# Performance work log

Measured on AMD Instinct MI355X. Metric: run time of the kernel, lower is better.

Reference implementation:

```python
import jax, jax.numpy as jnp
import numpy as np

N = 50000   # nodes
E = 800000  # edges (avg degree 16)
F = 128     # node_features


def setup_inputs() -> dict:
    key = jax.random.key(0)
    ks = jax.random.split(key, 10)
    s = 1.0 / np.sqrt(F)
    x = jax.random.normal(ks[0], (N, F), jnp.float32)
    edge_index = jax.random.randint(ks[1], (2, E), 0, N, dtype=jnp.int32)
    edge_weight = jax.random.uniform(ks[2], (E,), jnp.float32)
    # EvolveGCNO initial weight (glorot-ish) and GRU parameters (PyTorch layout)
    W0 = jax.random.uniform(ks[3], (F, F), jnp.float32, -s, s)
    W_ih = jax.random.uniform(ks[4], (3 * F, F), jnp.float32, -s, s)
    W_hh = jax.random.uniform(ks[5], (3 * F, F), jnp.float32, -s, s)
    b_ih = jax.random.uniform(ks[6], (3 * F,), jnp.float32, -s, s)
    b_hh = jax.random.uniform(ks[7], (3 * F,), jnp.float32, -s, s)
    # Linear(F, 1) head
    w_lin = jax.random.uniform(ks[8], (1, F), jnp.float32, -s, s)
    b_lin = jax.random.uniform(ks[9], (1,), jnp.float32, -s, s)
    return dict(x=x, edge_index=edge_index, edge_weight=edge_weight, W0=W0,
                W_ih=W_ih, W_hh=W_hh, b_ih=b_ih, b_hh=b_hh,
                w_lin=w_lin, b_lin=b_lin)


def _gru_evolve(W0, W_ih, W_hh, b_ih, b_hh):
    # GRU(input=W0, hidden=W0): seq_len=1, batch=F, feature=F (PyTorch gate order r,z,n)
    gi = W0 @ W_ih.T + b_ih  # [F, 3F]
    gh = W0 @ W_hh.T + b_hh  # [F, 3F]
    f = W0.shape[1]
    i_r, i_z, i_n = gi[:, :f], gi[:, f:2 * f], gi[:, 2 * f:]
    h_r, h_z, h_n = gh[:, :f], gh[:, f:2 * f], gh[:, 2 * f:]
    r = jax.nn.sigmoid(i_r + h_r)
    z = jax.nn.sigmoid(i_z + h_z)
    n = jnp.tanh(i_n + r * h_n)
    return (1.0 - z) * n + z * W0  # evolved weight [F, F]


def reference(x, edge_index, edge_weight, W0, W_ih, W_hh, b_ih, b_hh, w_lin, b_lin):
    n_nodes = x.shape[0]
    W = _gru_evolve(W0, W_ih, W_hh, b_ih, b_hh)
    # gcn_norm: add self loops (weight 1), symmetric D^-1/2 A D^-1/2
    loop = jnp.arange(n_nodes, dtype=edge_index.dtype)
    src = jnp.concatenate([edge_index[0], loop])
    dst = jnp.concatenate([edge_index[1], loop])
    w = jnp.concatenate([edge_weight, jnp.ones((n_nodes,), x.dtype)])
    deg = jax.ops.segment_sum(w, dst, num_segments=n_nodes)
    dinv = jnp.where(deg > 0, jax.lax.rsqrt(deg), 0.0)
    norm = dinv[src] * w * dinv[dst]  # [E+N]
    xw = x @ W  # [N, F]
    h = jax.ops.segment_sum(norm[:, None] * xw[src], dst, num_segments=n_nodes)
    h = jnp.tanh(h)
    return h @ w_lin.T + b_lin  # [N, 1]
```

## Files before the change

kernel.cpp:

```cpp
#include <hip/hip_runtime.h>
#include <hip/hip_bf16.h>
#include <math.h>

#define N_NODES 50000
#define N_EDGES 800000
#define FDIM 128
#define SCAN_BLOCKS 196
#define XW_BLOCKS 391

typedef unsigned int uint32;
typedef __attribute__((ext_vector_type(8))) __bf16 bf16x8;
typedef __attribute__((ext_vector_type(8))) short short8;
typedef __attribute__((ext_vector_type(16))) float f32x16;

#define FLAG_A 200
#define FLAG_B 201
#define SCANNED 256

__device__ inline unsigned short f2bf(float f) {
  unsigned int u = __float_as_uint(f);
  unsigned int r = u + 0x7fffu + ((u >> 16) & 1u);
  return (unsigned short)(r >> 16);
}

__global__ __launch_bounds__(384) void evolve_kernel(
    const float* __restrict__ W0, const float* __restrict__ Wih,
    const float* __restrict__ Whh, const float* __restrict__ bih,
    const float* __restrict__ bhh, float* __restrict__ W,
    int* __restrict__ cnt, int* __restrict__ part) {
  int i = blockIdx.x;
  int jj = threadIdx.x;
  int gid = i * 384 + jj;
  for (int j = gid; j < N_NODES; j += 128 * 384) cnt[j] = 0;
  if (gid == 0) part[FLAG_A] = 0;
  if (gid == 1) part[FLAG_B] = 0;

  __shared__ float w0s[FDIM];
  __shared__ float gis[3 * FDIM];
  __shared__ float ghs[3 * FDIM];
  if (jj < FDIM) w0s[jj] = W0[i * FDIM + jj];
  __syncthreads();
  float gi = bih[jj], gh = bhh[jj];
  const float4* wih4 = (const float4*)(Wih + jj * FDIM);
  const float4* whh4 = (const float4*)(Whh + jj * FDIM);
#pragma unroll 8
  for (int k = 0; k < FDIM / 4; k++) {
    float4 a = wih4[k];
    float4 b = whh4[k];
    float w0a = w0s[4 * k], w0b = w0s[4 * k + 1];
    float w0c = w0s[4 * k + 2], w0d = w0s[4 * k + 3];
    gi += a.x * w0a + a.y * w0b + a.z * w0c + a.w * w0d;
    gh += b.x * w0a + b.y * w0b + b.z * w0c + b.w * w0d;
  }
  gis[jj] = gi;
  ghs[jj] = gh;
  __syncthreads();
  if (jj < FDIM) {
    float r = 1.0f / (1.0f + expf(-(gis[jj] + ghs[jj])));
    float z = 1.0f / (1.0f + expf(-(gis[jj + FDIM] + ghs[jj + FDIM])));
    float nn = tanhf(gis[jj + 2 * FDIM] + r * ghs[jj + 2 * FDIM]);
    W[i * FDIM + jj] = (1.0f - z) * nn + z * w0s[jj];
  }
}

__global__ __launch_bounds__(256) void histxw_kernel(
    const int* __restrict__ ei, int* __restrict__ cnt, int* __restrict__ rank,
    const float* __restrict__ x, const float* __restrict__ W,
    unsigned short* __restrict__ y, int n) {
  __shared__ short Bs[16 * 128 * 8];
  int t = threadIdx.x;
  if (blockIdx.x >= XW_BLOCKS) {
    int idx = (blockIdx.x - XW_BLOCKS) * 256 + t;
    if (idx < N_EDGES) {
      int dst = ei[N_EDGES + idx];
      rank[idx] = atomicAdd(&cnt[dst], 1);
    }
    return;
  }
#pragma unroll
  for (int i = 0; i < 64; i++) {
    int idx = i * 256 + t;
    int k = idx >> 7, nn = idx & 127;
    Bs[(((k >> 3) << 7) + nn) * 8 + (k & 7)] = (short)f2bf(W[idx]);
  }
  __syncthreads();

  int lane = t & 63;
  int wid = blockIdx.x * 4 + (t >> 6);
  int tr = wid * 32;
  if (tr >= n) return;
  int m = lane & 31;
  int q2 = lane >> 5;

  int row = tr + m;
  if (row >= n) row = n - 1;
  const float* xr = x + (size_t)row * FDIM;

  bf16x8 a[8];
#pragma unroll
  for (int kc = 0; kc < 8; kc++) {
    int k0 = kc * 16 + q2 * 8;
    float4 p = *(const float4*)(xr + k0);
    float4 q = *(const float4*)(xr + k0 + 4);
    short8 s;
    s[0] = (short)f2bf(p.x); s[1] = (short)f2bf(p.y);
    s[2] = (short)f2bf(p.z); s[3] = (short)f2bf(p.w);
    s[4] = (short)f2bf(q.x); s[5] = (short)f2bf(q.y);
    s[6] = (short)f2bf(q.z); s[7] = (short)f2bf(q.w);
    a[kc] = __builtin_bit_cast(bf16x8, s);
  }

  f32x16 acc[4];
#pragma unroll
  for (int ct = 0; ct < 4; ct++) {
#pragma unroll
    for (int r = 0; r < 16; r++) acc[ct][r] = 0.0f;
  }
#pragma unroll
  for (int ct = 0; ct < 4; ct++) {
    int nn = ct * 32 + m;
#pragma unroll
    for (int kc = 0; kc < 8; kc++) {
      int kg = kc * 2 + q2;
      bf16x8 b = __builtin_bit_cast(
          bf16x8, *(const short8*)(Bs + (((kg << 7) + nn) << 3)));
      acc[ct] = __builtin_amdgcn_mfma_f32_32x32x16_bf16(a[kc], b, acc[ct], 0,
                                                        0, 0);
    }
  }

#pragma unroll
  for (int r = 0; r < 16; r++) {
    int rl = (r & 3) + ((r >> 2) << 3) + (q2 << 2);
    int rg = tr + rl;
    if (rg < n) {
#pragma unroll
      for (int ct = 0; ct < 4; ct++) {
        y[(size_t)rg * FDIM + ct * 32 + m] = f2bf(acc[ct][r]);
      }
    }
  }
}

__global__ __launch_bounds__(256) void scan_all_kernel(
    const int* __restrict__ cnt, int* __restrict__ part, int* __restrict__ offs,
    int n) {
  __shared__ int tmp[256];
  int t = threadIdx.x;
  int bid = blockIdx.x;
  int idx = bid * 256 + t;
  int v = (idx < n) ? cnt[idx] : 0;
  tmp[t] = v;
  __syncthreads();
#pragma unroll
  for (int off = 1; off < 256; off <<= 1) {
    int u = (t >= off) ? tmp[t - off] : 0;
    __syncthreads();
    tmp[t] += u;
    __syncthreads();
  }
  int local_excl = tmp[t] - v;
  int block_sum = tmp[255];
  if (t == 0) {
    __hip_atomic_store(&part[bid], block_sum, __ATOMIC_RELEASE,
                       __HIP_MEMORY_SCOPE_AGENT);
    __hip_atomic_fetch_add(&part[FLAG_A], 1, __ATOMIC_ACQ_REL,
                           __HIP_MEMORY_SCOPE_AGENT);
  }
  if (bid == 0) {
    if (t == 0) {
      while (__hip_atomic_load(&part[FLAG_A], __ATOMIC_ACQUIRE,
                               __HIP_MEMORY_SCOPE_AGENT) < SCAN_BLOCKS) {
        __builtin_amdgcn_s_sleep(1);
      }
    }
    __syncthreads();
    __shared__ int ps[256];
    int pv = (t < SCAN_BLOCKS)
                 ? __hip_atomic_load(&part[t], __ATOMIC_RELAXED,
                                     __HIP_MEMORY_SCOPE_AGENT)
                 : 0;
    ps[t] = pv;
    __syncthreads();
#pragma unroll
    for (int off = 1; off < 256; off <<= 1) {
      int u = (t >= off) ? ps[t - off] : 0;
      __syncthreads();
      ps[t] += u;
      __syncthreads();
    }
    if (t < SCAN_BLOCKS)
      __hip_atomic_store(&part[SCANNED + t], ps[t] - pv, __ATOMIC_RELAXED,
                         __HIP_MEMORY_SCOPE_AGENT);
    __syncthreads();
    if (t == 0)
      __hip_atomic_store(&part[FLAG_B], 1, __ATOMIC_RELEASE,
                         __HIP_MEMORY_SCOPE_AGENT);
  }
  if (t == 0) {
    while (__hip_atomic_load(&part[FLAG_B], __ATOMIC_ACQUIRE,
                             __HIP_MEMORY_SCOPE_AGENT) == 0) {
      __builtin_amdgcn_s_sleep(1);
    }
  }
  __syncthreads();
  int base = __hip_atomic_load(&part[SCANNED + bid], __ATOMIC_RELAXED,
                               __HIP_MEMORY_SCOPE_AGENT);
  int excl = base + local_excl;
  if (idx < n) offs[idx] = excl;
  if (idx == n - 1) offs[n] = excl + v;
}

__global__ void scatter_kernel(const int* __restrict__ ei,
                               const float* __restrict__ ew,
                               const int* __restrict__ offs,
                               const int* __restrict__ rank,
                               int2* __restrict__ csr, int e) {
  int idx = blockIdx.x * blockDim.x + threadIdx.x;
  if (idx < e) {
    int src = ei[idx];
    int dst = ei[N_EDGES + idx];
    int pos = offs[dst] + rank[idx];
    csr[pos] = make_int2(src, __float_as_int(ew[idx]));
  }
}

__global__ __launch_bounds__(256) void deg_dinv_kernel(
    const int2* __restrict__ csr, const int* __restrict__ offs,
    float* __restrict__ dinv, int n) {
  int i = blockIdx.x * blockDim.x + threadIdx.x;
  if (i >= n) return;
  int b = offs[i], e = offs[i + 1];
  float d = 1.0f;
  for (int j = b; j < e; j++) d += __int_as_float(csr[j].y);
  dinv[i] = (d > 0.0f) ? rsqrtf(d) : 0.0f;
}

__global__ __launch_bounds__(256) void gather_kernel(
    const uint32* __restrict__ yb, const int* __restrict__ offs,
    const int2* __restrict__ csr, const float* __restrict__ dinv,
    const float* __restrict__ wl, const float* __restrict__ bl,
    float* __restrict__ out, int n) {
  int wid = (int)((blockIdx.x * (size_t)blockDim.x + threadIdx.x) >> 6);
  int lane = threadIdx.x & 63;
  if (wid >= n) return;
  float di = dinv[wid];
  uint32 uv = yb[(size_t)wid * 64 + lane];
  float ax = di * __uint_as_float(uv << 16);
  float ay = di * __uint_as_float(uv & 0xffff0000u);
  int beg = offs[wid], end = offs[wid + 1];
  int e = beg;
  for (; e + 4 <= end; e += 4) {
    int2 c0 = csr[e];
    int2 c1 = csr[e + 1];
    int2 c2 = csr[e + 2];
    int2 c3 = csr[e + 3];
    uint32 u0 = yb[(size_t)c0.x * 64 + lane];
    uint32 u1 = yb[(size_t)c1.x * 64 + lane];
    uint32 u2 = yb[(size_t)c2.x * 64 + lane];
    uint32 u3 = yb[(size_t)c3.x * 64 + lane];
    float w0 = __int_as_float(c0.y) * dinv[c0.x];
    float w1 = __int_as_float(c1.y) * dinv[c1.x];
    float w2 = __int_as_float(c2.y) * dinv[c2.x];
    float w3 = __int_as_float(c3.y) * dinv[c3.x];
    ax += w0 * __uint_as_float(u0 << 16);
    ay += w0 * __uint_as_float(u0 & 0xffff0000u);
    ax += w1 * __uint_as_float(u1 << 16);
    ay += w1 * __uint_as_float(u1 & 0xffff0000u);
    ax += w2 * __uint_as_float(u2 << 16);
    ay += w2 * __uint_as_float(u2 & 0xffff0000u);
    ax += w3 * __uint_as_float(u3 << 16);
    ay += w3 * __uint_as_float(u3 & 0xffff0000u);
  }
  for (; e < end; e++) {
    int2 c = csr[e];
    uint32 u = yb[(size_t)c.x * 64 + lane];
    float wn = __int_as_float(c.y) * dinv[c.x];
    ax += wn * __uint_as_float(u << 16);
    ay += wn * __uint_as_float(u & 0xffff0000u);
  }
  float2 wv = ((const float2*)wl)[lane];
  float p = tanhf(di * ax) * wv.x + tanhf(di * ay) * wv.y;
#pragma unroll
  for (int o = 32; o > 0; o >>= 1) p += __shfl_down(p, o, 64);
  if (lane == 0) out[wid] = p + bl[0];
}

extern "C" void kernel_launch(void* const* d_in, const int* in_sizes, int n_in,
                              void* d_out, int out_size, void* d_ws,
                              size_t ws_size, hipStream_t stream) {
  const float* x = (const float*)d_in[0];
  const int* ei = (const int*)d_in[1];
  const float* ew = (const float*)d_in[2];
  const float* W0 = (const float*)d_in[3];
  const float* Wih = (const float*)d_in[4];
  const float* Whh = (const float*)d_in[5];
  const float* bih = (const float*)d_in[6];
  const float* bhh = (const float*)d_in[7];
  const float* wl = (const float*)d_in[8];
  const float* bl = (const float*)d_in[9];
  float* out = (float*)d_out;

  float* ws = (float*)d_ws;
  float* W_ev = ws;
  unsigned short* y = (unsigned short*)(W_ev + 16384);
  float* dinv = (float*)(y + (size_t)N_NODES * FDIM);
  int* cnt = (int*)(dinv + N_NODES);
  int* rank = cnt + N_NODES;
  int* offs = rank + N_EDGES;
  int2* csr = (int2*)(offs + 50004);
  int* part = (int*)(csr + N_EDGES);

  evolve_kernel<<<FDIM, 384, 0, stream>>>(W0, Wih, Whh, bih, bhh, W_ev, cnt,
                                          part);
  histxw_kernel<<<XW_BLOCKS + (N_EDGES + 255) / 256, 256, 0, stream>>>(
      ei, cnt, rank, x, W_ev, y, N_NODES);
  scan_all_kernel<<<SCAN_BLOCKS, 256, 0, stream>>>(cnt, part, offs, N_NODES);
  scatter_kernel<<<(N_EDGES + 255) / 256, 256, 0, stream>>>(ei, ew, offs, rank,
                                                            csr, N_EDGES);
  deg_dinv_kernel<<<(N_NODES + 255) / 256, 256, 0, stream>>>(csr, offs, dinv,
                                                             N_NODES);
  gather_kernel<<<(N_NODES * 64) / 256, 256, 0, stream>>>(
      (const uint32*)y, offs, csr, dinv, wl, bl, out, N_NODES);
}
```

Measured before the change: 213.7 us.

## Fuse degree, scan and scatter into one kernel and prenormalize CSR weights

Edge degrees are now accumulated with float atomics during the histogram pass. Scan and scatter are fused into one kernel behind a grid-wide barrier, and the deg_dinv kernel is removed. CSR weights are pre-multiplied by dinv[src], and the gather loads CSR entries cooperatively across the wavefront and broadcasts them with shuffles, so it no longer issues a dinv lookup per edge. The evolved weight is written already converted to bf16 in the MFMA layout, so histxw only does a vector copy. This removes two launches and redundant memory traffic, at the cost of float atomics that make degree summation order non-deterministic and a spin barrier that assumes all 196 scan blocks are resident at once.

```diff
diff --git a/kernel.cpp b/kernel.cpp
--- a/kernel.cpp
+++ b/kernel.cpp
@@ -15,6 +15,7 @@
 
 #define FLAG_A 200
 #define FLAG_B 201
+#define FLAG_C 202
 #define SCANNED 256
 
 __device__ inline unsigned short f2bf(float f) {
@@ -26,14 +27,16 @@
 __global__ __launch_bounds__(384) void evolve_kernel(
     const float* __restrict__ W0, const float* __restrict__ Wih,
     const float* __restrict__ Whh, const float* __restrict__ bih,
-    const float* __restrict__ bhh, float* __restrict__ W,
-    int* __restrict__ cnt, int* __restrict__ part) {
+    const float* __restrict__ bhh, unsigned short* __restrict__ Wbf,
+    int* __restrict__ cnt, float* __restrict__ degf, int* __restrict__ part) {
   int i = blockIdx.x;
   int jj = threadIdx.x;
   int gid = i * 384 + jj;
-  for (int j = gid; j < N_NODES; j += 128 * 384) cnt[j] = 0;
-  if (gid == 0) part[FLAG_A] = 0;
-  if (gid == 1) part[FLAG_B] = 0;
+  for (int j = gid; j < N_NODES; j += 128 * 384) {
+    cnt[j] = 0;
+    degf[j] = 0.0f;
+  }
+  if (gid < 3) part[FLAG_A + gid] = 0;
 
   __shared__ float w0s[FDIM];
   __shared__ float gis[3 * FDIM];
@@ -59,13 +62,15 @@
     float r = 1.0f / (1.0f + expf(-(gis[jj] + ghs[jj])));
     float z = 1.0f / (1.0f + expf(-(gis[jj + FDIM] + ghs[jj + FDIM])));
     float nn = tanhf(gis[jj + 2 * FDIM] + r * ghs[jj + 2 * FDIM]);
-    W[i * FDIM + jj] = (1.0f - z) * nn + z * w0s[jj];
+    float val = (1.0f - z) * nn + z * w0s[jj];
+    Wbf[((((i >> 3) << 7) + jj) << 3) + (i & 7)] = f2bf(val);
   }
 }
 
 __global__ __launch_bounds__(256) void histxw_kernel(
-    const int* __restrict__ ei, int* __restrict__ cnt, int* __restrict__ rank,
-    const float* __restrict__ x, const float* __restrict__ W,
+    const int* __restrict__ ei, const float* __restrict__ ew,
+    int* __restrict__ cnt, float* __restrict__ degf, int* __restrict__ rank,
+    const float* __restrict__ x, const unsigned short* __restrict__ Wbf,
     unsigned short* __restrict__ y, int n) {
   __shared__ short Bs[16 * 128 * 8];
   int t = threadIdx.x;
@@ -74,14 +79,13 @@
     if (idx < N_EDGES) {
       int dst = ei[N_EDGES + idx];
       rank[idx] = atomicAdd(&cnt[dst], 1);
+      unsafeAtomicAdd(&degf[dst], ew[idx]);
     }
     return;
   }
 #pragma unroll
-  for (int i = 0; i < 64; i++) {
-    int idx = i * 256 + t;
-    int k = idx >> 7, nn = idx & 127;
-    Bs[(((k >> 3) << 7) + nn) * 8 + (k & 7)] = (short)f2bf(W[idx]);
+  for (int i = 0; i < 8; i++) {
+    ((short8*)Bs)[i * 256 + t] = ((const short8*)Wbf)[i * 256 + t];
   }
   __syncthreads();
 
@@ -142,13 +146,17 @@
   }
 }
 
-__global__ __launch_bounds__(256) void scan_all_kernel(
-    const int* __restrict__ cnt, int* __restrict__ part, int* __restrict__ offs,
-    int n) {
+__global__ __launch_bounds__(256) void scan_scatter_kernel(
+    const int* __restrict__ cnt, const float* __restrict__ degf,
+    int* __restrict__ part, int* __restrict__ offs, float* __restrict__ dinv,
+    const int* __restrict__ ei, const float* __restrict__ ew,
+    const int* __restrict__ rank, int2* __restrict__ csr) {
   __shared__ int tmp[256];
   int t = threadIdx.x;
   int bid = blockIdx.x;
   int idx = bid * 256 + t;
+  int n = N_NODES;
+  if (idx < n) dinv[idx] = rsqrtf(degf[idx] + 1.0f);
   int v = (idx < n) ? cnt[idx] : 0;
   tmp[t] = v;
   __syncthreads();
@@ -209,31 +217,25 @@
   int excl = base + local_excl;
   if (idx < n) offs[idx] = excl;
   if (idx == n - 1) offs[n] = excl + v;
-}
-
-__global__ void scatter_kernel(const int* __restrict__ ei,
-                               const float* __restrict__ ew,
-                               const int* __restrict__ offs,
-                               const int* __restrict__ rank,
-                               int2* __restrict__ csr, int e) {
-  int idx = blockIdx.x * blockDim.x + threadIdx.x;
-  if (idx < e) {
-    int src = ei[idx];
-    int dst = ei[N_EDGES + idx];
-    int pos = offs[dst] + rank[idx];
-    csr[pos] = make_int2(src, __float_as_int(ew[idx]));
-  }
-}
-
-__global__ __launch_bounds__(256) void deg_dinv_kernel(
-    const int2* __restrict__ csr, const int* __restrict__ offs,
-    float* __restrict__ dinv, int n) {
-  int i = blockIdx.x * blockDim.x + threadIdx.x;
-  if (i >= n) return;
-  int b = offs[i], e = offs[i + 1];
-  float d = 1.0f;
-  for (int j = b; j < e; j++) d += __int_as_float(csr[j].y);
-  dinv[i] = (d > 0.0f) ? rsqrtf(d) : 0.0f;
+
+  __syncthreads();
+  if (t == 0) {
+    __hip_atomic_fetch_add(&part[FLAG_C], 1, __ATOMIC_ACQ_REL,
+                           __HIP_MEMORY_SCOPE_AGENT);
+    while (__hip_atomic_load(&part[FLAG_C], __ATOMIC_ACQUIRE,
+                             __HIP_MEMORY_SCOPE_AGENT) < SCAN_BLOCKS) {
+      __builtin_amdgcn_s_sleep(1);
+    }
+  }
+  __syncthreads();
+
+  for (int e = idx; e < N_EDGES; e += SCAN_BLOCKS * 256) {
+    int src = ei[e];
+    int dst = ei[N_EDGES + e];
+    int pos = offs[dst] + rank[e];
+    float wn = ew[e] * dinv[src];
+    csr[pos] = make_int2(src, __float_as_int(wn));
+  }
 }
 
 __global__ __launch_bounds__(256) void gather_kernel(
@@ -249,35 +251,41 @@
   float ax = di * __uint_as_float(uv << 16);
   float ay = di * __uint_as_float(uv & 0xffff0000u);
   int beg = offs[wid], end = offs[wid + 1];
-  int e = beg;
-  for (; e + 4 <= end; e += 4) {
-    int2 c0 = csr[e];
-    int2 c1 = csr[e + 1];
-    int2 c2 = csr[e + 2];
-    int2 c3 = csr[e + 3];
-    uint32 u0 = yb[(size_t)c0.x * 64 + lane];
-    uint32 u1 = yb[(size_t)c1.x * 64 + lane];
-    uint32 u2 = yb[(size_t)c2.x * 64 + lane];
-    uint32 u3 = yb[(size_t)c3.x * 64 + lane];
-    float w0 = __int_as_float(c0.y) * dinv[c0.x];
-    float w1 = __int_as_float(c1.y) * dinv[c1.x];
-    float w2 = __int_as_float(c2.y) * dinv[c2.x];
-    float w3 = __int_as_float(c3.y) * dinv[c3.x];
-    ax += w0 * __uint_as_float(u0 << 16);
-    ay += w0 * __uint_as_float(u0 & 0xffff0000u);
-    ax += w1 * __uint_as_float(u1 << 16);
-    ay += w1 * __uint_as_float(u1 & 0xffff0000u);
-    ax += w2 * __uint_as_float(u2 << 16);
-    ay += w2 * __uint_as_float(u2 & 0xffff0000u);
-    ax += w3 * __uint_as_float(u3 << 16);
-    ay += w3 * __uint_as_float(u3 & 0xffff0000u);
-  }
-  for (; e < end; e++) {
-    int2 c = csr[e];
-    uint32 u = yb[(size_t)c.x * 64 + lane];
-    float wn = __int_as_float(c.y) * dinv[c.x];
-    ax += wn * __uint_as_float(u << 16);
-    ay += wn * __uint_as_float(u & 0xffff0000u);
+  for (int base = beg; base < end; base += 64) {
+    int mm = end - base;
+    if (mm > 64) mm = 64;
+    int2 c = make_int2(0, 0);
+    if (lane < mm) c = csr[base + lane];
+    int j = 0;
+    for (; j + 4 <= mm; j += 4) {
+      int s0 = __shfl(c.x, j);
+      int s1 = __shfl(c.x, j + 1);
+      int s2 = __shfl(c.x, j + 2);
+      int s3 = __shfl(c.x, j + 3);
+      float w0 = __uint_as_float((uint32)__shfl(c.y, j));
+      float w1 = __uint_as_float((uint32)__shfl(c.y, j + 1));
+      float w2 = __uint_as_float((uint32)__shfl(c.y, j + 2));
+      float w3 = __uint_as_float((uint32)__shfl(c.y, j + 3));
+      uint32 u0 = yb[(size_t)s0 * 64 + lane];
+      uint32 u1 = yb[(size_t)s1 * 64 + lane];
+      uint32 u2 = yb[(size_t)s2 * 64 + lane];
+      uint32 u3 = yb[(size_t)s3 * 64 + lane];
+      ax += w0 * __uint_as_float(u0 << 16);
+      ay += w0 * __uint_as_float(u0 & 0xffff0000u);
+      ax += w1 * __uint_as_float(u1 << 16);
+      ay += w1 * __uint_as_float(u1 & 0xffff0000u);
+      ax += w2 * __uint_as_float(u2 << 16);
+      ay += w2 * __uint_as_float(u2 & 0xffff0000u);
+      ax += w3 * __uint_as_float(u3 << 16);
+      ay += w3 * __uint_as_float(u3 & 0xffff0000u);
+    }
+    for (; j < mm; j++) {
+      int s = __shfl(c.x, j);
+      float wn = __uint_as_float((uint32)__shfl(c.y, j));
+      uint32 u = yb[(size_t)s * 64 + lane];
+      ax += wn * __uint_as_float(u << 16);
+      ay += wn * __uint_as_float(u & 0xffff0000u);
+    }
   }
   float2 wv = ((const float2*)wl)[lane];
   float p = tanhf(di * ax) * wv.x + tanhf(di * ay) * wv.y;
@@ -301,25 +309,22 @@
   const float* bl = (const float*)d_in[9];
   float* out = (float*)d_out;
 
-  float* ws = (float*)d_ws;
-  float* W_ev = ws;
-  unsigned short* y = (unsigned short*)(W_ev + 16384);
+  unsigned short* Wbf = (unsigned short*)d_ws;
+  unsigned short* y = Wbf + 16384;
   float* dinv = (float*)(y + (size_t)N_NODES * FDIM);
-  int* cnt = (int*)(dinv + N_NODES);
+  float* degf = dinv + N_NODES;
+  int* cnt = (int*)(degf + N_NODES);
   int* rank = cnt + N_NODES;
   int* offs = rank + N_EDGES;
   int2* csr = (int2*)(offs + 50004);
   int* part = (int*)(csr + N_EDGES);
 
-  evolve_kernel<<<FDIM, 384, 0, stream>>>(W0, Wih, Whh, bih, bhh, W_ev, cnt,
-                                          part);
+  evolve_kernel<<<FDIM, 384, 0, stream>>>(W0, Wih, Whh, bih, bhh, Wbf, cnt,
+                                          degf, part);
   histxw_kernel<<<XW_BLOCKS + (N_EDGES + 255) / 256, 256, 0, stream>>>(
-      ei, cnt, rank, x, W_ev, y, N_NODES);
-  scan_all_kernel<<<SCAN_BLOCKS, 256, 0, stream>>>(cnt, part, offs, N_NODES);
-  scatter_kernel<<<(N_EDGES + 255) / 256, 256, 0, stream>>>(ei, ew, offs, rank,
-                                                            csr, N_EDGES);
-  deg_dinv_kernel<<<(N_NODES + 255) / 256, 256, 0, stream>>>(csr, offs, dinv,
-                                                             N_NODES);
+      ei, ew, cnt, degf, rank, x, Wbf, y, N_NODES);
+  scan_scatter_kernel<<<SCAN_BLOCKS, 256, 0, stream>>>(cnt, degf, part, offs,
+                                                       dinv, ei, ew, rank, csr);
   gather_kernel<<<(N_NODES * 64) / 256, 256, 0, stream>>>(
       (const uint32*)y, offs, csr, dinv, wl, bl, out, N_NODES);
 }
```

Measured after the change: 253.3 us. +18.5%, slower.

## Replicate histogram counters and prepack evolved weight as bf16 in MFMA layout

Applied to the files above, without the earlier changes.

Splits the per-node edge counter into 8 replicas selected by block index, with each thread handling four edges via int4 loads and tagging its rank with the replica id. The scan sums the replicas and writes per-replica base offsets back, which scatter uses for placement. The evolve kernel now writes W directly as bf16 in the MFMA-friendly layout, and the xw blocks load it in two half-tiles, removing the per-block fp32-to-bf16 conversion and halving LDS use. This targets atomic contention on hot destinations and redundant conversion work, at the cost of 8x counter memory and the extra zeroing that goes with it.

```diff
diff --git a/kernel.cpp b/kernel.cpp
--- a/kernel.cpp
+++ b/kernel.cpp
@@ -7,6 +7,8 @@
 #define FDIM 128
 #define SCAN_BLOCKS 196
 #define XW_BLOCKS 391
+#define HIST_BLOCKS 782
+#define NREP 8
 
 typedef unsigned int uint32;
 typedef __attribute__((ext_vector_type(8))) __bf16 bf16x8;
@@ -26,14 +28,13 @@
 __global__ __launch_bounds__(384) void evolve_kernel(
     const float* __restrict__ W0, const float* __restrict__ Wih,
     const float* __restrict__ Whh, const float* __restrict__ bih,
-    const float* __restrict__ bhh, float* __restrict__ W,
-    int* __restrict__ cnt, int* __restrict__ part) {
+    const float* __restrict__ bhh, unsigned short* __restrict__ Wbf,
+    int* __restrict__ cnt_r, int* __restrict__ part) {
   int i = blockIdx.x;
   int jj = threadIdx.x;
   int gid = i * 384 + jj;
-  for (int j = gid; j < N_NODES; j += 128 * 384) cnt[j] = 0;
-  if (gid == 0) part[FLAG_A] = 0;
-  if (gid == 1) part[FLAG_B] = 0;
+  for (int j = gid; j < NREP * N_NODES; j += 128 * 384) cnt_r[j] = 0;
+  if (gid < 2) part[FLAG_A + gid] = 0;
 
   __shared__ float w0s[FDIM];
   __shared__ float gis[3 * FDIM];
@@ -59,36 +60,34 @@
     float r = 1.0f / (1.0f + expf(-(gis[jj] + ghs[jj])));
     float z = 1.0f / (1.0f + expf(-(gis[jj + FDIM] + ghs[jj + FDIM])));
     float nn = tanhf(gis[jj + 2 * FDIM] + r * ghs[jj + 2 * FDIM]);
-    W[i * FDIM + jj] = (1.0f - z) * nn + z * w0s[jj];
+    float val = (1.0f - z) * nn + z * w0s[jj];
+    Wbf[((((i >> 3) << 7) + jj) << 3) + (i & 7)] = f2bf(val);
   }
 }
 
 __global__ __launch_bounds__(256) void histxw_kernel(
-    const int* __restrict__ ei, int* __restrict__ cnt, int* __restrict__ rank,
-    const float* __restrict__ x, const float* __restrict__ W,
+    const int* __restrict__ ei, int* __restrict__ cnt_r, int* __restrict__ rank,
+    const float* __restrict__ x, const unsigned short* __restrict__ Wbf,
     unsigned short* __restrict__ y, int n) {
-  __shared__ short Bs[16 * 128 * 8];
+  __shared__ short Bs[8192];
   int t = threadIdx.x;
   if (blockIdx.x >= XW_BLOCKS) {
-    int idx = (blockIdx.x - XW_BLOCKS) * 256 + t;
-    if (idx < N_EDGES) {
-      int dst = ei[N_EDGES + idx];
-      rank[idx] = atomicAdd(&cnt[dst], 1);
+    int rep = blockIdx.x & (NREP - 1);
+    int e0 = (blockIdx.x - XW_BLOCKS) * 1024 + t * 4;
+    if (e0 < N_EDGES) {
+      int4 d4 = *(const int4*)(ei + N_EDGES + e0);
+      int tag = rep << 24;
+      int r0 = atomicAdd(&cnt_r[d4.x * NREP + rep], 1);
+      int r1 = atomicAdd(&cnt_r[d4.y * NREP + rep], 1);
+      int r2 = atomicAdd(&cnt_r[d4.z * NREP + rep], 1);
+      int r3 = atomicAdd(&cnt_r[d4.w * NREP + rep], 1);
+      *(int4*)(rank + e0) = make_int4(tag | r0, tag | r1, tag | r2, tag | r3);
     }
     return;
   }
-#pragma unroll
-  for (int i = 0; i < 64; i++) {
-    int idx = i * 256 + t;
-    int k = idx >> 7, nn = idx & 127;
-    Bs[(((k >> 3) << 7) + nn) * 8 + (k & 7)] = (short)f2bf(W[idx]);
-  }
-  __syncthreads();
-
   int lane = t & 63;
   int wid = blockIdx.x * 4 + (t >> 6);
   int tr = wid * 32;
-  if (tr >= n) return;
   int m = lane & 31;
   int q2 = lane >> 5;
 
@@ -116,16 +115,29 @@
 #pragma unroll
     for (int r = 0; r < 16; r++) acc[ct][r] = 0.0f;
   }
-#pragma unroll
-  for (int ct = 0; ct < 4; ct++) {
-    int nn = ct * 32 + m;
-#pragma unroll
-    for (int kc = 0; kc < 8; kc++) {
-      int kg = kc * 2 + q2;
-      bf16x8 b = __builtin_bit_cast(
-          bf16x8, *(const short8*)(Bs + (((kg << 7) + nn) << 3)));
-      acc[ct] = __builtin_amdgcn_mfma_f32_32x32x16_bf16(a[kc], b, acc[ct], 0,
-                                                        0, 0);
+
+#pragma unroll
+  for (int h = 0; h < 2; h++) {
+    __syncthreads();
+#pragma unroll
+    for (int i = 0; i < 4; i++) {
+      int li = i * 256 + t;
+      ((short8*)Bs)[li] =
+          ((const short8*)Wbf)[((li >> 6) << 7) + (h << 6) + (li & 63)];
+    }
+    __syncthreads();
+#pragma unroll
+    for (int cti = 0; cti < 2; cti++) {
+      int ct = h * 2 + cti;
+      int nnl = cti * 32 + m;
+#pragma unroll
+      for (int kc = 0; kc < 8; kc++) {
+        int kg = kc * 2 + q2;
+        bf16x8 b = __builtin_bit_cast(bf16x8,
+                                      ((const short8*)Bs)[(kg << 6) + nnl]);
+        acc[ct] = __builtin_amdgcn_mfma_f32_32x32x16_bf16(a[kc], b, acc[ct],
+                                                          0, 0, 0);
+      }
     }
   }
 
@@ -143,13 +155,22 @@
 }
 
 __global__ __launch_bounds__(256) void scan_all_kernel(
-    const int* __restrict__ cnt, int* __restrict__ part, int* __restrict__ offs,
+    int* __restrict__ cnt_r, int* __restrict__ part, int* __restrict__ offs,
     int n) {
   __shared__ int tmp[256];
   int t = threadIdx.x;
   int bid = blockIdx.x;
   int idx = bid * 256 + t;
-  int v = (idx < n) ? cnt[idx] : 0;
+  int c[NREP];
+  int v = 0;
+  if (idx < n) {
+    int4 a = *(const int4*)(cnt_r + idx * NREP);
+    int4 b = *(const int4*)(cnt_r + idx * NREP + 4);
+    c[0] = a.x; c[1] = a.y; c[2] = a.z; c[3] = a.w;
+    c[4] = b.x; c[5] = b.y; c[6] = b.z; c[7] = b.w;
+#pragma unroll
+    for (int r = 0; r < NREP; r++) v += c[r];
+  }
   tmp[t] = v;
   __syncthreads();
 #pragma unroll
@@ -207,20 +228,37 @@
   int base = __hip_atomic_load(&part[SCANNED + bid], __ATOMIC_RELAXED,
                                __HIP_MEMORY_SCOPE_AGENT);
   int excl = base + local_excl;
-  if (idx < n) offs[idx] = excl;
+  if (idx < n) {
+    offs[idx] = excl;
+    int run = excl;
+    int4 o0, o1;
+    o0.x = run; run += c[0];
+    o0.y = run; run += c[1];
+    o0.z = run; run += c[2];
+    o0.w = run; run += c[3];
+    o1.x = run; run += c[4];
+    o1.y = run; run += c[5];
+    o1.z = run; run += c[6];
+    o1.w = run;
+    *(int4*)(cnt_r + idx * NREP) = o0;
+    *(int4*)(cnt_r + idx * NREP + 4) = o1;
+  }
   if (idx == n - 1) offs[n] = excl + v;
 }
 
 __global__ void scatter_kernel(const int* __restrict__ ei,
                                const float* __restrict__ ew,
-                               const int* __restrict__ offs,
+                               const int* __restrict__ base_r,
                                const int* __restrict__ rank,
                                int2* __restrict__ csr, int e) {
   int idx = blockIdx.x * blockDim.x + threadIdx.x;
   if (idx < e) {
     int src = ei[idx];
     int dst = ei[N_EDGES + idx];
-    int pos = offs[dst] + rank[idx];
+    int rw = rank[idx];
+    int rep = ((uint32)rw) >> 24;
+    int loc = rw & 0xFFFFFF;
+    int pos = base_r[dst * NREP + rep] + loc;
     csr[pos] = make_int2(src, __float_as_int(ew[idx]));
   }
 }
@@ -301,23 +339,23 @@
   const float* bl = (const float*)d_in[9];
   float* out = (float*)d_out;
 
-  float* ws = (float*)d_ws;
-  float* W_ev = ws;
-  unsigned short* y = (unsigned short*)(W_ev + 16384);
+  unsigned short* Wbf = (unsigned short*)d_ws;
+  unsigned short* y = Wbf + 16384;
   float* dinv = (float*)(y + (size_t)N_NODES * FDIM);
-  int* cnt = (int*)(dinv + N_NODES);
-  int* rank = cnt + N_NODES;
+  int* cnt_r = (int*)(dinv + N_NODES);
+  int* rank = cnt_r + NREP * N_NODES;
   int* offs = rank + N_EDGES;
   int2* csr = (int2*)(offs + 50004);
   int* part = (int*)(csr + N_EDGES);
 
-  evolve_kernel<<<FDIM, 384, 0, stream>>>(W0, Wih, Whh, bih, bhh, W_ev, cnt,
+  evolve_kernel<<<FDIM, 384, 0, stream>>>(W0, Wih, Whh, bih, bhh, Wbf, cnt_r,
                                           part);
-  histxw_kernel<<<XW_BLOCKS + (N_EDGES + 255) / 256, 256, 0, stream>>>(
-      ei, cnt, rank, x, W_ev, y, N_NODES);
-  scan_all_kernel<<<SCAN_BLOCKS, 256, 0, stream>>>(cnt, part, offs, N_NODES);
-  scatter_kernel<<<(N_EDGES + 255) / 256, 256, 0, stream>>>(ei, ew, offs, rank,
-                                                            csr, N_EDGES);
+  histxw_kernel<<<XW_BLOCKS + HIST_BLOCKS, 256, 0, stream>>>(ei, cnt_r, rank,
+                                                             x, Wbf, y,
+                                                             N_NODES);
+  scan_all_kernel<<<SCAN_BLOCKS, 256, 0, stream>>>(cnt_r, part, offs, N_NODES);
+  scatter_kernel<<<(N_EDGES + 255) / 256, 256, 0, stream>>>(ei, ew, cnt_r,
+                                                            rank, csr, N_EDGES);
   deg_dinv_kernel<<<(N_NODES + 255) / 256, 256, 0, stream>>>(csr, offs, dinv,
                                                              N_NODES);
   gather_kernel<<<(N_NODES * 64) / 256, 256, 0, stream>>>(
```

New measurement: 216.3 us. No clear change (+1.2%).
